# Performance work log

Hardware: AMD Instinct MI355X
Metric: run time of the kernel (lower is better)

## Reference

```python
import jax, jax.numpy as jnp
import numpy as np

B, T, I, H = 64, 512, 1024, 1024


def setup_inputs() -> dict:
    key = jax.random.key(0)
    k1, k2, k3, k4 = jax.random.split(key, 4)
    scale_ih = (6.0 / (H + I)) ** 0.5  # xavier_uniform bound
    scale_hh = (6.0 / (H + H)) ** 0.5
    return {
        "x": jax.random.normal(k1, (B, T, I), dtype=jnp.float32),
        "h0": jax.random.normal(k2, (1, B, H), dtype=jnp.float32),
        "W_ih": jax.random.uniform(k3, (H, I), dtype=jnp.float32, minval=-scale_ih, maxval=scale_ih),
        "b_ih": jnp.zeros((H,), dtype=jnp.float32),
        "W_hh": jax.random.uniform(k4, (H, H), dtype=jnp.float32, minval=-scale_hh, maxval=scale_hh),
        "b_hh": jnp.zeros((H,), dtype=jnp.float32),
    }


def reference(x, h0, W_ih, b_ih, W_hh, b_hh):
    # h_t = tanh(x_t @ W_ih^T + b_ih + h_{t-1} @ W_hh^T + b_hh)
    # Precompute the input projection for all timesteps (same math, batched GEMM).
    xp = jnp.einsum("bti,hi->tbh", x, W_ih) + b_ih  # [T,B,H]
    h = h0[0]  # [B,H]

    def step(h, xp_t):
        h_new = jnp.tanh(xp_t + h @ W_hh.T + b_hh)
        return h_new, h_new

    _, ys = jax.lax.scan(step, h, xp)  # ys: [T,B,H]
    return jnp.transpose(ys, (1, 0, 2))  # [B,T,H]
```

## Files before the change

### kernel.cpp

```cpp
#include <hip/hip_runtime.h>
#include <hip/hip_bf16.h>

#define BB_   64
#define TT_   512
#define II_   1024
#define HH_   1024

typedef _Float16 half8  __attribute__((ext_vector_type(8)));
typedef _Float16 half4v __attribute__((ext_vector_type(4)));
typedef float    f32x4  __attribute__((ext_vector_type(4)));

__device__ __forceinline__ float fast_tanh(float x) {
    float t = fminf(fmaxf(x, -16.f), 16.f);
    float e = __builtin_amdgcn_exp2f(t * 2.885390082f);
    return 1.f - 2.f * __builtin_amdgcn_rcpf(e + 1.f);
}

__device__ __forceinline__ void gload_lds16(const void* g, void* l) {
    __builtin_amdgcn_global_load_lds(
        (const __attribute__((address_space(1))) unsigned*)g,
        (__attribute__((address_space(3))) unsigned*)l, 16, 0, 0);
}

__global__ __launch_bounds__(256) void cvt_f16(const float4* __restrict__ src,
                                               half4v* __restrict__ dst, int n4) {
    int i = blockIdx.x * blockDim.x + threadIdx.x;
    const int stride = gridDim.x * blockDim.x;
    for (; i < n4; i += stride) {
        const float4 v = src[i];
        half4v h = { (_Float16)v.x, (_Float16)v.y, (_Float16)v.z, (_Float16)v.w };
        dst[i] = h;
    }
}

__global__ __launch_bounds__(256) void gemm_xp_f16(const _Float16* __restrict__ xh,
                                                   const _Float16* __restrict__ Wh,
                                                   const float* __restrict__ bih,
                                                   float* __restrict__ out) {
    __shared__ alignas(16) _Float16 As[128 * 64];
    __shared__ alignas(16) _Float16 Bs[128 * 64];

    const int tid  = threadIdx.x;
    const int xcd  = blockIdx.x & 7;
    const int idx  = blockIdx.x >> 3;
    const int bm   = xcd + 8 * (idx >> 3);
    const int bn   = idx & 7;
    const int M0   = bm * 128, N0 = bn * 128;
    const int lane = tid & 63, w = tid >> 6;
    const int wm   = (w & 1) * 64, wn = (w >> 1) * 64;
    const int ro   = lane & 15, q = lane >> 4;

    const int srow  = w * 8 + (lane >> 3);
    const int schunk = (lane & 7) ^ ((lane >> 3) & 7);
    _Float16* ldsA = As + (size_t)(w * 8) * 64 + (size_t)(lane & 63) * 0 + (size_t)((lane >> 3)) * 64 + (lane & 7) * 8;
    _Float16* ldsB = Bs + (size_t)srow * 64 + (lane & 7) * 8;
    ldsA = As + (size_t)srow * 64 + (lane & 7) * 8;

    const f32x4 zero4 = {0.f, 0.f, 0.f, 0.f};
    f32x4 acc[4][4];
    #pragma unroll
    for (int i = 0; i < 4; ++i)
        #pragma unroll
        for (int j = 0; j < 4; ++j) acc[i][j] = zero4;

    for (int kk = 0; kk < 16; ++kk) {
        const int k0 = kk * 64;
        #pragma unroll
        for (int ir = 0; ir < 4; ++ir) {
            const int row = ir * 32 + srow;
            gload_lds16(xh + (size_t)(M0 + row) * II_ + k0 + schunk * 8,
                        ldsA + ir * 32 * 64);
            gload_lds16(Wh + (size_t)(N0 + row) * II_ + k0 + schunk * 8,
                        ldsB + ir * 32 * 64);
        }
        __syncthreads();

        half8 a[2][4], b[2][4];
        #pragma unroll
        for (int sub = 0; sub < 2; ++sub)
            #pragma unroll
            for (int i = 0; i < 4; ++i) {
                const int Ra = wm + i * 16 + ro;
                const int Rb = wn + i * 16 + ro;
                a[sub][i] = *(const half8*)(As + Ra * 64 + (((sub * 4 + q) ^ (Ra & 7)) * 8));
                b[sub][i] = *(const half8*)(Bs + Rb * 64 + (((sub * 4 + q) ^ (Rb & 7)) * 8));
            }
        #pragma unroll
        for (int sub = 0; sub < 2; ++sub)
            #pragma unroll
            for (int i = 0; i < 4; ++i)
                #pragma unroll
                for (int j = 0; j < 4; ++j)
                    acc[i][j] = __builtin_amdgcn_mfma_f32_16x16x32_f16(a[sub][i], b[sub][j], acc[i][j], 0, 0, 0);
        __syncthreads();
    }

    #pragma unroll
    for (int j = 0; j < 4; ++j) {
        const int col = N0 + wn + j * 16 + ro;
        const float bias = bih[col];
        #pragma unroll
        for (int i = 0; i < 4; ++i) {
            #pragma unroll
            for (int r = 0; r < 4; ++r) {
                const int rowg = M0 + wm + i * 16 + q * 4 + r;
                out[(size_t)rowg * HH_ + col] = acc[i][j][r] + bias;
            }
        }
    }
}

__global__ __launch_bounds__(256) void gemm_xp(const float* __restrict__ x,
                                               const float* __restrict__ Wih,
                                               const float* __restrict__ bih,
                                               float* __restrict__ out) {
    __shared__ alignas(16) _Float16 As[2][128 * 40];
    __shared__ alignas(16) _Float16 Bs[2][128 * 40];

    const int tid  = threadIdx.x;
    const int xcd  = blockIdx.x & 7;
    const int idx  = blockIdx.x >> 3;
    const int bm   = xcd + 8 * (idx >> 3);
    const int bn   = idx & 7;
    const int M0   = bm * 128, N0 = bn * 128;
    const int lane = tid & 63, w = tid >> 6;
    const int wm   = (w & 1) * 64, wn = (w >> 1) * 64;
    const int ro   = lane & 15, q = lane >> 4;
    const int sr   = tid >> 3, sc = tid & 7;

    const f32x4 zero4 = {0.f, 0.f, 0.f, 0.f};
    f32x4 acc[4][4];
    #pragma unroll
    for (int i = 0; i < 4; ++i)
        #pragma unroll
        for (int j = 0; j < 4; ++j) acc[i][j] = zero4;

    for (int kk = 0; kk < 16; ++kk) {
        #pragma unroll
        for (int sub = 0; sub < 2; ++sub) {
            const int k0 = kk * 64 + sub * 32;
            #pragma unroll
            for (int ir = 0; ir < 4; ++ir) {
                const int row = ir * 32 + sr;
                const float4 av = *(const float4*)(x   + (size_t)(M0 + row) * II_ + k0 + sc * 4);
                const float4 bv = *(const float4*)(Wih + (size_t)(N0 + row) * II_ + k0 + sc * 4);
                half4v ah = { (_Float16)av.x, (_Float16)av.y, (_Float16)av.z, (_Float16)av.w };
                half4v bh = { (_Float16)bv.x, (_Float16)bv.y, (_Float16)bv.z, (_Float16)bv.w };
                *(half4v*)(As[sub] + row * 40 + sc * 4) = ah;
                *(half4v*)(Bs[sub] + row * 40 + sc * 4) = bh;
            }
        }
        __syncthreads();

        half8 a[2][4], b[2][4];
        #pragma unroll
        for (int sub = 0; sub < 2; ++sub)
            #pragma unroll
            for (int i = 0; i < 4; ++i) {
                a[sub][i] = *(const half8*)(As[sub] + (wm + i * 16 + ro) * 40 + q * 8);
                b[sub][i] = *(const half8*)(Bs[sub] + (wn + i * 16 + ro) * 40 + q * 8);
            }
        #pragma unroll
        for (int sub = 0; sub < 2; ++sub)
            #pragma unroll
            for (int i = 0; i < 4; ++i)
                #pragma unroll
                for (int j = 0; j < 4; ++j)
                    acc[i][j] = __builtin_amdgcn_mfma_f32_16x16x32_f16(a[sub][i], b[sub][j], acc[i][j], 0, 0, 0);
        __syncthreads();
    }

    #pragma unroll
    for (int j = 0; j < 4; ++j) {
        const int col = N0 + wn + j * 16 + ro;
        const float bias = bih[col];
        #pragma unroll
        for (int i = 0; i < 4; ++i) {
            #pragma unroll
            for (int r = 0; r < 4; ++r) {
                const int rowg = M0 + wm + i * 16 + q * 4 + r;
                out[(size_t)rowg * HH_ + col] = acc[i][j][r] + bias;
            }
        }
    }
}

__global__ __launch_bounds__(256, 1) void rnn_steps(const float* __restrict__ Whh,
                                                    const float* __restrict__ bhh,
                                                    const float* __restrict__ h0,
                                                    float* __restrict__ out,
                                                    unsigned* __restrict__ comm) {
    __shared__ alignas(16) _Float16 hbuf[2][5][1032];

    const int tid  = threadIdx.x;
    const int lane = tid & 63;
    const int w    = tid >> 6;
    const int g    = blockIdx.x >> 4;
    const int wg   = blockIdx.x & 15;
    const int b0   = g * 4;
    const int j0   = wg * 64;
    const int ro   = lane & 15, q = lane >> 4;
    const int arow = (ro < 4) ? ro : 4;
    const int bat  = lane >> 4;
    const int colw = j0 + w * 16 + (lane & 15);

    half8 wf[4][8];
    {
        const float* wrow = Whh + (size_t)(j0 + w * 16 + ro) * HH_;
        #pragma unroll
        for (int kq = 0; kq < 4; ++kq) {
            #pragma unroll
            for (int ks = 0; ks < 8; ++ks) {
                const int kc = kq * 256 + ks * 32 + q * 8;
                const float4 w0 = *(const float4*)(wrow + kc);
                const float4 w1 = *(const float4*)(wrow + kc + 4);
                half8 hv;
                hv[0] = (_Float16)w0.x; hv[1] = (_Float16)w0.y;
                hv[2] = (_Float16)w0.z; hv[3] = (_Float16)w0.w;
                hv[4] = (_Float16)w1.x; hv[5] = (_Float16)w1.y;
                hv[6] = (_Float16)w1.z; hv[7] = (_Float16)w1.w;
                wf[kq][ks] = hv;
            }
        }
    }
    const float bhh_r = bhh[colw];

    for (int i = tid; i < 1032; i += 256) {
        hbuf[0][4][i] = (_Float16)0.f;
        hbuf[1][4][i] = (_Float16)0.f;
    }

    const f32x4 zero4 = {0.f, 0.f, 0.f, 0.f};

    #define TAGMSK_ 0xFFFF0000FFFF0000ull
    #define TAGOK_(v) ((((v) ^ pat) & TAGMSK_) == 0)

    for (int s = 0; s < TT_; ++s) {
        const int slot = s & 1;

        const float xpv = out[((size_t)(b0 + bat) * TT_ + s) * HH_ + colw];

        unsigned* dstw = (unsigned*)(&hbuf[slot][w][0]);
        if (s == 0) {
            const float2* hrow = (const float2*)(h0 + (size_t)(b0 + w) * HH_);
            #pragma unroll
            for (int c = 0; c < 8; ++c) {
                const float2 hv = hrow[c * 64 + lane];
                union { _Float16 h[2]; unsigned u; } pk;
                pk.h[0] = (_Float16)hv.x; pk.h[1] = (_Float16)hv.y;
                dstw[c * 64 + lane] = pk.u;
            }
        } else {
            const unsigned long long pat =
                ((unsigned long long)(unsigned)s << 48) |
                ((unsigned long long)(unsigned)s << 16);
            const unsigned long long* sp = (const unsigned long long*)
                (comm + (size_t)slot * (BB_ * HH_) + (size_t)(b0 + w) * HH_);
            unsigned long long v0, v1, v2, v3, v4, v5, v6, v7;
            bool ok = false;
            while (!ok) {
                v0 = __hip_atomic_load(sp + 0 * 64 + lane, __ATOMIC_RELAXED, __HIP_MEMORY_SCOPE_AGENT);
                v1 = __hip_atomic_load(sp + 1 * 64 + lane, __ATOMIC_RELAXED, __HIP_MEMORY_SCOPE_AGENT);
                v2 = __hip_atomic_load(sp + 2 * 64 + lane, __ATOMIC_RELAXED, __HIP_MEMORY_SCOPE_AGENT);
                v3 = __hip_atomic_load(sp + 3 * 64 + lane, __ATOMIC_RELAXED, __HIP_MEMORY_SCOPE_AGENT);
                v4 = __hip_atomic_load(sp + 4 * 64 + lane, __ATOMIC_RELAXED, __HIP_MEMORY_SCOPE_AGENT);
                v5 = __hip_atomic_load(sp + 5 * 64 + lane, __ATOMIC_RELAXED, __HIP_MEMORY_SCOPE_AGENT);
                v6 = __hip_atomic_load(sp + 6 * 64 + lane, __ATOMIC_RELAXED, __HIP_MEMORY_SCOPE_AGENT);
                v7 = __hip_atomic_load(sp + 7 * 64 + lane, __ATOMIC_RELAXED, __HIP_MEMORY_SCOPE_AGENT);
                bool o = true;
                o &= TAGOK_(v0); o &= TAGOK_(v1); o &= TAGOK_(v2); o &= TAGOK_(v3);
                o &= TAGOK_(v4); o &= TAGOK_(v5); o &= TAGOK_(v6); o &= TAGOK_(v7);
                ok = o;
            }
            #define PACK_(x) ((unsigned)((x) & 0xffffull) | (((unsigned)((x) >> 32)) << 16))
            dstw[0 * 64 + lane] = PACK_(v0);
            dstw[1 * 64 + lane] = PACK_(v1);
            dstw[2 * 64 + lane] = PACK_(v2);
            dstw[3 * 64 + lane] = PACK_(v3);
            dstw[4 * 64 + lane] = PACK_(v4);
            dstw[5 * 64 + lane] = PACK_(v5);
            dstw[6 * 64 + lane] = PACK_(v6);
            dstw[7 * 64 + lane] = PACK_(v7);
            #undef PACK_
        }
        __syncthreads();

        f32x4 acc[4] = {zero4, zero4, zero4, zero4};
        const _Float16* abase = &hbuf[slot][0][0] + (size_t)arow * 1032;
        #pragma unroll
        for (int kq = 0; kq < 4; ++kq) {
            #pragma unroll
            for (int ks = 0; ks < 8; ++ks) {
                const half8 a = *(const half8*)(abase + kq * 256 + ks * 32 + q * 8);
                acc[kq] = __builtin_amdgcn_mfma_f32_16x16x32_f16(a, wf[kq][ks], acc[kq], 0, 0, 0);
            }
        }

        const f32x4 sum = acc[0] + acc[1] + acc[2] + acc[3];
        const float t0 = __shfl(sum[0], lane & 15);
        const float t1 = __shfl(sum[1], lane & 15);
        const float t2 = __shfl(sum[2], lane & 15);
        const float t3 = __shfl(sum[3], lane & 15);
        const float val = (bat == 0) ? t0 : (bat == 1) ? t1 : (bat == 2) ? t2 : t3;

        const float hnew = fast_tanh(xpv + bhh_r + val);

        union { _Float16 h; unsigned short us; } cv; cv.h = (_Float16)hnew;
        const unsigned word = ((unsigned)(s + 1) << 16) | (unsigned)cv.us;
        __hip_atomic_store(comm + (size_t)((s + 1) & 1) * (BB_ * HH_)
                                + (size_t)(b0 + bat) * HH_ + colw,
                           word, __ATOMIC_RELAXED, __HIP_MEMORY_SCOPE_AGENT);

        out[((size_t)(b0 + bat) * TT_ + s) * HH_ + colw] = hnew;
    }
    #undef TAGOK_
    #undef TAGMSK_
}

extern "C" void kernel_launch(void* const* d_in, const int* in_sizes, int n_in,
                              void* d_out, int out_size, void* d_ws, size_t ws_size,
                              hipStream_t stream) {
    (void)in_sizes; (void)n_in; (void)out_size;

    const float* x   = (const float*)d_in[0];
    const float* h0  = (const float*)d_in[1];
    const float* Wih = (const float*)d_in[2];
    const float* bih = (const float*)d_in[3];
    const float* Whh = (const float*)d_in[4];
    const float* bhh = (const float*)d_in[5];
    float* out = (float*)d_out;

    const size_t COMMB = 2 * (size_t)(BB_ * HH_) * sizeof(unsigned);
    const size_t WFB   = (size_t)HH_ * II_ * sizeof(_Float16);
    const size_t XFB   = (size_t)BB_ * TT_ * II_ * sizeof(_Float16);
    unsigned* comm = (unsigned*)d_ws;

    if (ws_size >= COMMB + WFB + XFB) {
        _Float16* Wh = (_Float16*)((char*)d_ws + COMMB);
        _Float16* xh = (_Float16*)((char*)d_ws + COMMB + WFB);
        cvt_f16<<<512, 256, 0, stream>>>((const float4*)Wih, (half4v*)Wh,
                                         HH_ * II_ / 4);
        cvt_f16<<<2048, 256, 0, stream>>>((const float4*)x, (half4v*)xh,
                                          BB_ * TT_ * II_ / 4);
        gemm_xp_f16<<<2048, 256, 0, stream>>>(xh, Wh, bih, out);
    } else {
        gemm_xp<<<2048, 256, 0, stream>>>(x, Wih, bih, out);
    }
    rnn_steps<<<256, 256, 0, stream>>>(Whh, bhh, h0, out, comm);
}
```

Before: 1.416 ms.

## Double-buffer LDS tiles in f16 input-projection GEMM with K=32 stages

Reworks the input-projection GEMM to use two LDS buffers with a K-step of 32 instead of a single K=64 buffer. The next tile's global-to-LDS loads are issued before computing on the current tile. This is meant to overlap memory latency with MFMA work and drop one barrier per iteration. In exchange there are twice as many loop iterations, each with less compute, and the XOR swizzle is narrowed to 4 chunks, which may raise LDS bank conflicts.

```diff
diff --git a/kernel.cpp b/kernel.cpp
--- a/kernel.cpp
+++ b/kernel.cpp
@@ -37,8 +37,8 @@
                                                    const _Float16* __restrict__ Wh,
                                                    const float* __restrict__ bih,
                                                    float* __restrict__ out) {
-    __shared__ alignas(16) _Float16 As[128 * 64];
-    __shared__ alignas(16) _Float16 Bs[128 * 64];
+    __shared__ alignas(16) _Float16 As[2][128 * 32];
+    __shared__ alignas(16) _Float16 Bs[2][128 * 32];
 
     const int tid  = threadIdx.x;
     const int xcd  = blockIdx.x & 7;
@@ -50,11 +50,21 @@
     const int wm   = (w & 1) * 64, wn = (w >> 1) * 64;
     const int ro   = lane & 15, q = lane >> 4;
 
-    const int srow  = w * 8 + (lane >> 3);
-    const int schunk = (lane & 7) ^ ((lane >> 3) & 7);
-    _Float16* ldsA = As + (size_t)(w * 8) * 64 + (size_t)(lane & 63) * 0 + (size_t)((lane >> 3)) * 64 + (lane & 7) * 8;
-    _Float16* ldsB = Bs + (size_t)srow * 64 + (lane & 7) * 8;
-    ldsA = As + (size_t)srow * 64 + (lane & 7) * 8;
+    const int srow   = w * 16 + (lane >> 2);
+    const int schunk = (lane & 3) ^ ((lane >> 2) & 3);
+    const size_t soff = (size_t)srow * 32 + (size_t)(lane & 3) * 8;
+
+    #define STAGE_(buf, kk_) do {                                              \
+        const int k0_ = (kk_) * 32;                                            \
+        gload_lds16(xh + (size_t)(M0 + srow) * II_ + k0_ + schunk * 8,         \
+                    &As[buf][0] + soff);                                       \
+        gload_lds16(xh + (size_t)(M0 + 64 + srow) * II_ + k0_ + schunk * 8,    \
+                    &As[buf][0] + soff + 64 * 32);                             \
+        gload_lds16(Wh + (size_t)(N0 + srow) * II_ + k0_ + schunk * 8,         \
+                    &Bs[buf][0] + soff);                                       \
+        gload_lds16(Wh + (size_t)(N0 + 64 + srow) * II_ + k0_ + schunk * 8,    \
+                    &Bs[buf][0] + soff + 64 * 32);                             \
+    } while (0)
 
     const f32x4 zero4 = {0.f, 0.f, 0.f, 0.f};
     f32x4 acc[4][4];
@@ -63,37 +73,31 @@
         #pragma unroll
         for (int j = 0; j < 4; ++j) acc[i][j] = zero4;
 
-    for (int kk = 0; kk < 16; ++kk) {
-        const int k0 = kk * 64;
-        #pragma unroll
-        for (int ir = 0; ir < 4; ++ir) {
-            const int row = ir * 32 + srow;
-            gload_lds16(xh + (size_t)(M0 + row) * II_ + k0 + schunk * 8,
-                        ldsA + ir * 32 * 64);
-            gload_lds16(Wh + (size_t)(N0 + row) * II_ + k0 + schunk * 8,
-                        ldsB + ir * 32 * 64);
-        }
+    STAGE_(0, 0);
+    __syncthreads();
+
+    int cur = 0;
+    for (int kk = 0; kk < 32; ++kk) {
+        if (kk < 31) STAGE_(cur ^ 1, kk + 1);
+
+        half8 a[4], b[4];
+        #pragma unroll
+        for (int i = 0; i < 4; ++i) {
+            const int Ra = wm + i * 16 + ro;
+            const int Rb = wn + i * 16 + ro;
+            a[i] = *(const half8*)(&As[cur][0] + Ra * 32 + ((q ^ (Ra & 3)) * 8));
+            b[i] = *(const half8*)(&Bs[cur][0] + Rb * 32 + ((q ^ (Rb & 3)) * 8));
+        }
+        #pragma unroll
+        for (int i = 0; i < 4; ++i)
+            #pragma unroll
+            for (int j = 0; j < 4; ++j)
+                acc[i][j] = __builtin_amdgcn_mfma_f32_16x16x32_f16(a[i], b[j], acc[i][j], 0, 0, 0);
+
         __syncthreads();
-
-        half8 a[2][4], b[2][4];
-        #pragma unroll
-        for (int sub = 0; sub < 2; ++sub)
-            #pragma unroll
-            for (int i = 0; i < 4; ++i) {
-                const int Ra = wm + i * 16 + ro;
-                const int Rb = wn + i * 16 + ro;
-                a[sub][i] = *(const half8*)(As + Ra * 64 + (((sub * 4 + q) ^ (Ra & 7)) * 8));
-                b[sub][i] = *(const half8*)(Bs + Rb * 64 + (((sub * 4 + q) ^ (Rb & 7)) * 8));
-            }
-        #pragma unroll
-        for (int sub = 0; sub < 2; ++sub)
-            #pragma unroll
-            for (int i = 0; i < 4; ++i)
-                #pragma unroll
-                for (int j = 0; j < 4; ++j)
-                    acc[i][j] = __builtin_amdgcn_mfma_f32_16x16x32_f16(a[sub][i], b[sub][j], acc[i][j], 0, 0, 0);
-        __syncthreads();
-    }
+        cur ^= 1;
+    }
+    #undef STAGE_
 
     #pragma unroll
     for (int j = 0; j < 4; ++j) {
```

Measured after the change: 1.425 ms. No clear change (+0.7%).
